# Optimization experiments

Measured on AMD Instinct MI355X. Metric: run time of the kernel, lower is better.

Reference implementation:

```python
import jax, jax.numpy as jnp
import numpy as np

B, C, N, H = 4, 512, 2048, 8
D = C // H  # per-head depth = 64
EPS = 1e-5


def conv1x1(x, W, b):
    # x: [B, Cin, N], W: [Cout, Cin], b: [Cout]
    return jnp.einsum('oc,bcn->bon', W, x) + b[None, :, None]


def instance_norm(x):
    # normalize over length dim per (batch, channel), no affine
    mu = jnp.mean(x, axis=-1, keepdims=True)
    var = jnp.var(x, axis=-1, keepdims=True)
    return (x - mu) * jax.lax.rsqrt(var + EPS)


def _pipeline(src, tgt, Wq, bq, Wk, bk, Wv, bv, Wm, bm):
    # query from src, key/value from tgt; reshape C -> (D outer, H inner)
    q = conv1x1(src, Wq, bq).reshape(B, D, H, N)
    k = conv1x1(tgt, Wk, bk).reshape(B, D, H, N)
    v = conv1x1(tgt, Wv, bv).reshape(B, D, H, N)
    scores = jnp.einsum('bdhn,bdhm->bhnm', q, k) / jnp.sqrt(jnp.float32(D))
    probs = jax.nn.softmax(scores, axis=-1)
    out = jnp.einsum('bhnm,bdhm->bdhn', probs, v).reshape(B, C, N)
    return conv1x1(out, Wm, bm)


def _mlp(x, W1, b1, W2, b2):
    h = conv1x1(x, W1, b1)
    h = jax.nn.relu(instance_norm(h))
    return conv1x1(h, W2, b2)


def setup_inputs() -> dict:
    key = jax.random.key(0)
    ks = jax.random.split(key, 8)
    s = 0.02
    return {
        'source_features': jax.random.normal(ks[0], (B, C, N), jnp.float32),
        'target_features': jax.random.normal(ks[1], (B, C, N), jnp.float32),
        'Wq': jax.random.normal(ks[2], (C, C), jnp.float32) * s,
        'bq': jnp.zeros((C,), jnp.float32),
        'Wk': jax.random.normal(ks[3], (C, C), jnp.float32) * s,
        'bk': jnp.zeros((C,), jnp.float32),
        'Wv': jax.random.normal(ks[4], (C, C), jnp.float32) * s,
        'bv': jnp.zeros((C,), jnp.float32),
        'Wm': jax.random.normal(ks[5], (C, C), jnp.float32) * s,
        'bm': jnp.zeros((C,), jnp.float32),
        'W1': jax.random.normal(ks[6], (2 * C, 2 * C), jnp.float32) * s,
        'b1': jnp.zeros((2 * C,), jnp.float32),
        'W2': jax.random.normal(ks[7], (C, 2 * C), jnp.float32) * s,
        'b2': jnp.zeros((C,), jnp.float32),
    }


def reference(source_features, target_features, Wq, bq, Wk, bk, Wv, bv, Wm, bm, W1, b1, W2, b2):
    src, tgt = source_features, target_features
    # source update uses ORIGINAL target features
    src_att = _pipeline(src, tgt, Wq, bq, Wk, bk, Wv, bv, Wm, bm)
    src = src + _mlp(jnp.concatenate([src, src_att], axis=1), W1, b1, W2, b2)
    # target update uses the UPDATED source features (in-place semantics of original)
    tgt_att = _pipeline(tgt, src, Wq, bq, Wk, bk, Wv, bv, Wm, bm)
    tgt = tgt + _mlp(jnp.concatenate([tgt, tgt_att], axis=1), W1, b1, W2, b2)
    return src, tgt
```

## Files before the change

### kernel.cpp

```cpp
#include <hip/hip_runtime.h>

#define NN 2048
#define CC 512
#define BB 4
#define HH 8
#define DD 64
#define SCALE 0.18033688011112043f

typedef unsigned short u16;
typedef __attribute__((ext_vector_type(8))) short bf16x8;
typedef __attribute__((ext_vector_type(4))) float f32x4;

extern "C" __device__ float __ocml_exp2_f32(float);

__device__ inline u16 f2b(float x) {
    unsigned u = __builtin_bit_cast(unsigned, x);
    u += 0x7fffu + ((u >> 16) & 1u);
    return (u16)(u >> 16);
}
__device__ inline float b2f(u16 h) {
    unsigned u = ((unsigned)h) << 16;
    return __builtin_bit_cast(float, u);
}

#define GLD16(g, l) __builtin_amdgcn_global_load_lds( \
    (const __attribute__((address_space(1))) unsigned int*)(g), \
    (__attribute__((address_space(3))) unsigned int*)(l), 16, 0, 0)

template<int JT>
__device__ __forceinline__ void gemm_core_t(
    const u16* __restrict__ Xa, const u16* __restrict__ Xb, int Ca, int K,
    const u16* __restrict__ Wt, size_t rowBase,
    u16* As, u16* Bs, f32x4 (&acc)[4][JT])
{
    constexpr int OT = JT * 32;
    const int tid = threadIdx.x;
    const int lane = tid & 63, w = tid >> 6;
    const int quad = lane >> 4, l16 = lane & 15;
    const int wrow = w & 1, wcol = w >> 1;
    const int arow = lane >> 2, aseg = lane & 3;

    for (int k0 = 0; k0 < K; k0 += 32) {
        const u16* Xs; int Crow, cc;
        if (k0 < Ca) { Xs = Xa; Crow = Ca; cc = k0; }
        else         { Xs = Xb; Crow = K - Ca; cc = k0 - Ca; }
#pragma unroll
        for (int i = 0; i < 2; ++i) {
            int rl = w * 32 + i * 16 + arow;
            int la = __builtin_amdgcn_readfirstlane((w * 32 + i * 16) * 32);
            GLD16(Xs + (rowBase + rl) * (size_t)Crow + cc + aseg * 8, (char*)As + (size_t)la * 2);
        }
#pragma unroll
        for (int i = 0; i < OT / 64; ++i) {
            int rl = w * (OT / 4) + i * 16 + arow;
            int la = __builtin_amdgcn_readfirstlane((w * (OT / 4) + i * 16) * 32);
            GLD16(Wt + (size_t)rl * K + k0 + aseg * 8, (char*)Bs + (size_t)la * 2);
        }
        __syncthreads();
        bf16x8 av[4], bv[JT];
#pragma unroll
        for (int i = 0; i < 4; ++i)
            av[i] = *(const bf16x8*)&As[(wrow * 64 + i * 16 + l16) * 32 + quad * 8];
#pragma unroll
        for (int jj = 0; jj < JT; ++jj)
            bv[jj] = *(const bf16x8*)&Bs[(wcol * JT * 16 + jj * 16 + l16) * 32 + quad * 8];
#pragma unroll
        for (int i = 0; i < 4; ++i)
#pragma unroll
            for (int jj = 0; jj < JT; ++jj)
                acc[i][jj] = __builtin_amdgcn_mfma_f32_16x16x32_bf16(av[i], bv[jj], acc[i][jj], 0, 0, 0);
        __syncthreads();
    }
}

template<int JT>
__device__ __forceinline__ void gemm_epilogue_t(
    f32x4 (&acc)[4][JT], const float* __restrict__ bias, int mode,
    int b, int n0, int o0, int Cout,
    const float* __restrict__ res, float* __restrict__ outF, u16* __restrict__ outB)
{
    const int tid = threadIdx.x;
    const int lane = tid & 63, w = tid >> 6;
    const int quad = lane >> 4, l16 = lane & 15;
    const int wrow = w & 1, wcol = w >> 1;
    const size_t bN = (size_t)b * NN;
    const int nb0 = n0 + wrow * 64, ob0 = o0 + wcol * JT * 16;

    if (mode == 0) {
#pragma unroll
        for (int j = 0; j < JT; ++j) {
            int o = ob0 + j * 16 + l16;
            float bs = bias[o];
#pragma unroll
            for (int i = 0; i < 4; ++i)
#pragma unroll
                for (int r = 0; r < 4; ++r) {
                    int n = nb0 + i * 16 + quad * 4 + r;
                    outB[(bN + n) * Cout + o] = f2b(acc[i][j][r] + bs);
                }
        }
    } else if (mode == 1) {
#pragma unroll
        for (int j = 0; j < JT; ++j) {
            int o = ob0 + j * 16 + l16;
            float bs = bias[o];
            int h = o >> 6, d = o & 63;
#pragma unroll
            for (int i = 0; i < 4; ++i) {
                int n = nb0 + i * 16 + quad * 4;
                ushort4 pk;
                pk.x = f2b(acc[i][j][0] + bs); pk.y = f2b(acc[i][j][1] + bs);
                pk.z = f2b(acc[i][j][2] + bs); pk.w = f2b(acc[i][j][3] + bs);
                *(ushort4*)&outB[(((size_t)b * HH + h) * DD + d) * NN + n] = pk;
            }
        }
    } else {
#pragma unroll
        for (int j = 0; j < JT; ++j) {
            int o = ob0 + j * 16 + l16;
            float bs = bias[o];
#pragma unroll
            for (int i = 0; i < 4; ++i) {
                int n = nb0 + i * 16 + quad * 4;
                size_t ad = ((size_t)b * Cout + o) * NN + n;
                float4 rv = *(const float4*)&res[ad];
                float4 yv;
                yv.x = acc[i][j][0] + bs + rv.x;
                yv.y = acc[i][j][1] + bs + rv.y;
                yv.z = acc[i][j][2] + bs + rv.z;
                yv.w = acc[i][j][3] + bs + rv.w;
                *(float4*)&outF[ad] = yv;
                if (mode == 2) {
                    outB[(bN + n + 0) * Cout + o] = f2b(yv.x);
                    outB[(bN + n + 1) * Cout + o] = f2b(yv.y);
                    outB[(bN + n + 2) * Cout + o] = f2b(yv.z);
                    outB[(bN + n + 3) * Cout + o] = f2b(yv.w);
                }
            }
        }
    }
}

template<int JT>
__global__ __launch_bounds__(256, (JT == 2 ? 4 : 3)) void gemm_bf16_t(
    const u16* __restrict__ Wb, const float* __restrict__ bias,
    const u16* __restrict__ Xa, const u16* __restrict__ Xb,
    int Ca, int K, int Cout,
    const float* __restrict__ res, float* __restrict__ outF,
    u16* __restrict__ outB, int mode)
{
    __shared__ u16 As[128 * 32];
    __shared__ u16 Bs[JT * 32 * 32];
    const int b = blockIdx.z, n0 = blockIdx.x * 128, o0 = blockIdx.y * (JT * 32);
    f32x4 acc[4][JT] = {};
    gemm_core_t<JT>(Xa, Xb, Ca, K, Wb + (size_t)o0 * K, (size_t)b * NN + n0, As, Bs, acc);
    gemm_epilogue_t<JT>(acc, bias, mode, b, n0, o0, Cout, res, outF, outB);
}

__global__ __launch_bounds__(256, 3) void gemm_qkv(
    const u16* __restrict__ WQ, const float* __restrict__ bQ,
    const u16* __restrict__ XQ, u16* __restrict__ outQ,
    const u16* __restrict__ WK, const float* __restrict__ bK, u16* __restrict__ outK,
    const u16* __restrict__ WV, const float* __restrict__ bV, u16* __restrict__ outV,
    const u16* __restrict__ XKV)
{
    __shared__ u16 As[128 * 32];
    __shared__ u16 Bs[128 * 32];
    const int yb = blockIdx.y;
    const u16* W; const float* bias; const u16* X; u16* outB; int mode, o0;
    if (yb < 4)      { o0 = yb * 128;       W = WQ; bias = bQ; X = XQ;  outB = outQ; mode = 0; }
    else if (yb < 8) { o0 = (yb - 4) * 128; W = WK; bias = bK; X = XKV; outB = outK; mode = 0; }
    else             { o0 = (yb - 8) * 128; W = WV; bias = bV; X = XKV; outB = outV; mode = 1; }
    const int b = blockIdx.z, n0 = blockIdx.x * 128;
    f32x4 acc[4][4] = {};
    gemm_core_t<4>(X, nullptr, 512, 512, W + (size_t)o0 * 512, (size_t)b * NN + n0, As, Bs, acc);
    gemm_epilogue_t<4>(acc, bias, mode, b, n0, o0, 512, nullptr, nullptr, outB);
}

__global__ __launch_bounds__(256, 4) void attn(
    const u16* __restrict__ Qg, const u16* __restrict__ Kg,
    const u16* __restrict__ Vg, u16* __restrict__ Og)
{
    __shared__ __align__(16) u16 Ks[64 * 64];
    __shared__ __align__(16) u16 Vt[64 * 64];
    __shared__ __align__(16) u16 Ps[64 * 64];
    const int tid = threadIdx.x;
    const int lane = tid & 63, w = tid >> 6;
    const int quad = lane >> 4, l16 = lane & 15;
    const int id = blockIdx.x;
    const int xcd = id & 7, jj = id >> 3;
    const int bh = xcd * 4 + (jj >> 5), nb = jj & 31;
    const int b = bh >> 3, h = bh & 7;
    const int n0 = nb * 64, wn0 = w * 16;
    const size_t qkBase = ((size_t)b * NN) * CC + h * DD;
    const size_t vBase  = (((size_t)b * HH + h) * DD) * NN;
    const int r8 = lane >> 3, seg = lane & 7;
    const int lk = l16 & 7;

    bf16x8 qf[2];
    {
        int n = n0 + wn0 + l16;
#pragma unroll
        for (int ks = 0; ks < 2; ++ks)
            qf[ks] = *(const bf16x8*)&Qg[qkBase + (size_t)n * CC + ks * 32 + quad * 8];
    }

    const short oneb = 0x3F80;
    const bf16x8 ones = {oneb, oneb, oneb, oneb, oneb, oneb, oneb, oneb};
    f32x4 oa[4] = {};
    f32x4 lacc = {};

    for (int m0 = 0; m0 < NN; m0 += 64) {
#pragma unroll
        for (int it = 0; it < 2; ++it) {
            int rowb = w * 16 + it * 8;
            int segp = seg ^ r8;
            GLD16(&Kg[qkBase + (size_t)(m0 + rowb + r8) * CC + segp * 8], &Ks[rowb * 64]);
            GLD16(&Vg[vBase + (size_t)(rowb + r8) * NN + m0 + segp * 8], &Vt[rowb * 64]);
        }
        __syncthreads();

        f32x4 st[4] = {};
#pragma unroll
        for (int ks = 0; ks < 2; ++ks) {
            bf16x8 ak[4];
#pragma unroll
            for (int rt = 0; rt < 4; ++rt)
                ak[rt] = *(const bf16x8*)&Ks[(rt * 16 + l16) * 64 + ((ks * 4 + quad) ^ lk) * 8];
#pragma unroll
            for (int rt = 0; rt < 4; ++rt)
                st[rt] = __builtin_amdgcn_mfma_f32_16x16x32_bf16(ak[rt], qf[ks], st[rt], 0, 0, 0);
        }

        {
            int nrow = wn0 + l16;
#pragma unroll
            for (int rt = 0; rt < 4; ++rt) {
                unsigned u0 = __builtin_bit_cast(unsigned, __ocml_exp2_f32(st[rt][0]));
                unsigned u1 = __builtin_bit_cast(unsigned, __ocml_exp2_f32(st[rt][1]));
                unsigned u2 = __builtin_bit_cast(unsigned, __ocml_exp2_f32(st[rt][2]));
                unsigned u3 = __builtin_bit_cast(unsigned, __ocml_exp2_f32(st[rt][3]));
                uint2 t;
                t.x = __builtin_amdgcn_perm(u1, u0, 0x07060302u);
                t.y = __builtin_amdgcn_perm(u3, u2, 0x07060302u);
                int g = (rt * 2 + (quad >> 1)) ^ lk;
                *(uint2*)&Ps[nrow * 64 + g * 8 + (quad & 1) * 4] = t;
            }
        }

#pragma unroll
        for (int ks = 0; ks < 2; ++ks) {
            bf16x8 pa = *(const bf16x8*)&Ps[(wn0 + l16) * 64 + ((ks * 4 + quad) ^ lk) * 8];
            bf16x8 vb[4];
#pragma unroll
            for (int ct = 0; ct < 4; ++ct)
                vb[ct] = *(const bf16x8*)&Vt[(ct * 16 + l16) * 64 + ((ks * 4 + quad) ^ lk) * 8];
#pragma unroll
            for (int ct = 0; ct < 4; ++ct)
                oa[ct] = __builtin_amdgcn_mfma_f32_16x16x32_bf16(pa, vb[ct], oa[ct], 0, 0, 0);
            lacc = __builtin_amdgcn_mfma_f32_16x16x32_bf16(pa, ones, lacc, 0, 0, 0);
        }
        __syncthreads();
    }

#pragma unroll
    for (int r = 0; r < 4; ++r) {
        float li = 1.f / lacc[r];
        int n = n0 + wn0 + quad * 4 + r;
#pragma unroll
        for (int ct = 0; ct < 4; ++ct)
            Og[qkBase + (size_t)n * CC + ct * 16 + l16] = f2b(oa[ct][r] * li);
    }
}

__global__ __launch_bounds__(256) void transpose_cvt(
    const float* __restrict__ X, u16* __restrict__ Y)
{
    __shared__ float T[64][65];
    const int tid = threadIdx.x;
    const int n0 = blockIdx.x * 64, c0 = blockIdx.y * 64, b = blockIdx.z;
    const int rr = tid >> 4, cc4 = tid & 15;
#pragma unroll
    for (int p = 0; p < 4; ++p) {
        int cl = p * 16 + rr;
        float4 v = *(const float4*)&X[((size_t)b * CC + c0 + cl) * NN + n0 + cc4 * 4];
        T[cl][cc4 * 4 + 0] = v.x; T[cl][cc4 * 4 + 1] = v.y;
        T[cl][cc4 * 4 + 2] = v.z; T[cl][cc4 * 4 + 3] = v.w;
    }
    __syncthreads();
#pragma unroll
    for (int p = 0; p < 4; ++p) {
        int nl = p * 16 + rr;
        ushort4 pk;
        pk.x = f2b(T[cc4 * 4 + 0][nl]);
        pk.y = f2b(T[cc4 * 4 + 1][nl]);
        pk.z = f2b(T[cc4 * 4 + 2][nl]);
        pk.w = f2b(T[cc4 * 4 + 3][nl]);
        *(ushort4*)&Y[((size_t)b * NN + n0 + nl) * CC + c0 + cc4 * 4] = pk;
    }
}

__global__ __launch_bounds__(256) void prep_weights(
    const float* __restrict__ Wq, const float* __restrict__ Wk,
    const float* __restrict__ Wv, const float* __restrict__ Wm,
    const float* __restrict__ W1, const float* __restrict__ W2,
    u16* oQ, u16* oK, u16* oV, u16* oM, u16* o1, u16* o2)
{
    const float* W; u16* o; int rows, cols, perm; float sc = 1.f;
    switch (blockIdx.z) {
        case 0: W = Wq; o = oQ; rows = 512;  cols = 512;  perm = 1; sc = SCALE; break;
        case 1: W = Wk; o = oK; rows = 512;  cols = 512;  perm = 1; break;
        case 2: W = Wv; o = oV; rows = 512;  cols = 512;  perm = 1; break;
        case 3: W = Wm; o = oM; rows = 512;  cols = 512;  perm = 2; break;
        case 4: W = W1; o = o1; rows = 1024; cols = 1024; perm = 0; break;
        default: W = W2; o = o2; rows = 512; cols = 1024; perm = 0; break;
    }
    int c = blockIdx.x * 256 + threadIdx.x;
    int r = blockIdx.y;
    if (r >= rows || c >= cols) return;
    int sr = r, scol = c;
    if (perm == 1) sr = (r & 63) * 8 + (r >> 6);
    else if (perm == 2) scol = (c & 63) * 8 + (c >> 6);
    o[(size_t)r * cols + c] = f2b(W[(size_t)sr * cols + scol] * sc);
}

__global__ void prep_bias(const float* __restrict__ bq, const float* __restrict__ bk,
                          const float* __restrict__ bv,
                          float* oq, float* ok, float* ov)
{
    int i = blockIdx.x * 256 + threadIdx.x;
    int y = blockIdx.y;
    const float* s = (y == 0) ? bq : (y == 1) ? bk : bv;
    float* o = (y == 0) ? oq : (y == 1) ? ok : ov;
    float v = s[(i & 63) * 8 + (i >> 6)];
    if (y == 0) v *= SCALE;
    o[i] = v;
}

__global__ __launch_bounds__(256) void inorm_p1(
    const u16* __restrict__ X, float* __restrict__ Ssum, float* __restrict__ Ssq)
{
    __shared__ float rs[4][64], rq[4][64];
    const int tid = threadIdx.x;
    const int cl = tid & 63, g = tid >> 6;
    const int c = blockIdx.x * 64 + cl;
    const int b = blockIdx.y, nz = blockIdx.z;
    float s = 0.f, q = 0.f;
    size_t base = ((size_t)b * NN + nz * 256 + g * 64) * 1024 + c;
#pragma unroll 4
    for (int i = 0; i < 64; ++i) {
        float x = b2f(X[base + (size_t)i * 1024]);
        s += x; q += x * x;
    }
    rs[g][cl] = s; rq[g][cl] = q;
    __syncthreads();
    if (g == 0) {
        s = rs[0][cl] + rs[1][cl] + rs[2][cl] + rs[3][cl];
        q = rq[0][cl] + rq[1][cl] + rq[2][cl] + rq[3][cl];
        atomicAdd(&Ssum[b * 1024 + c], s);
        atomicAdd(&Ssq[b * 1024 + c], q);
    }
}

__global__ __launch_bounds__(256) void inorm_p2(
    u16* __restrict__ X, const float* __restrict__ Ssum, const float* __restrict__ Ssq)
{
    const int tid = threadIdx.x;
    const int cl = tid & 63, g = tid >> 6;
    const int c = blockIdx.x * 64 + cl;
    const int b = blockIdx.y, nz = blockIdx.z;
    float mean = Ssum[b * 1024 + c] * (1.f / NN);
    float var  = Ssq[b * 1024 + c] * (1.f / NN) - mean * mean;
    float rstd = rsqrtf(fmaxf(var, 0.f) + 1e-5f);
    size_t base = ((size_t)b * NN + nz * 256 + g * 64) * 1024 + c;
#pragma unroll 4
    for (int i = 0; i < 64; ++i) {
        float x = b2f(X[base + (size_t)i * 1024]);
        x = (x - mean) * rstd;
        X[base + (size_t)i * 1024] = f2b(fmaxf(x, 0.f));
    }
}

extern "C" void kernel_launch(void* const* d_in, const int* in_sizes, int n_in,
                              void* d_out, int out_size, void* d_ws, size_t ws_size,
                              hipStream_t stream)
{
    (void)in_sizes; (void)n_in; (void)out_size; (void)ws_size;
    const float* src = (const float*)d_in[0];
    const float* tgt = (const float*)d_in[1];
    const float* Wq = (const float*)d_in[2];  const float* bq = (const float*)d_in[3];
    const float* Wk = (const float*)d_in[4];  const float* bk = (const float*)d_in[5];
    const float* Wv = (const float*)d_in[6];  const float* bv = (const float*)d_in[7];
    const float* Wm = (const float*)d_in[8];  const float* bm = (const float*)d_in[9];
    const float* W1 = (const float*)d_in[10]; const float* b1 = (const float*)d_in[11];
    const float* W2 = (const float*)d_in[12]; const float* b2 = (const float*)d_in[13];

    char* w = (char*)d_ws;
    u16* WQp = (u16*)(w);
    u16* WKp = (u16*)(w + (512u << 10));
    u16* WVp = (u16*)(w + (1u << 20));
    u16* WMp = (u16*)(w + (3u << 19));
    u16* W1b = (u16*)(w + (2u << 20));
    u16* W2b = (u16*)(w + (4u << 20));
    float* BQp = (float*)(w + (5u << 20));
    float* BKp = BQp + 512;
    float* BVp = BQp + 1024;
    float* STS = BQp + 1536;
    float* STQ = STS + 4096;
    u16* X0 = (u16*)(w + ( 6u << 20));
    u16* X1 = (u16*)(w + (14u << 20));
    u16* B0 = (u16*)(w + (22u << 20));
    u16* B1 = (u16*)(w + (30u << 20));
    u16* B2 = (u16*)(w + (38u << 20));
    u16* B3 = (u16*)(w + (46u << 20));

    float* out = (float*)d_out;
    const size_t R = (size_t)BB * CC * NN;
    dim3 blk(256);

    prep_weights<<<dim3(4, 1024, 6), blk, 0, stream>>>(Wq, Wk, Wv, Wm, W1, W2,
                                                       WQp, WKp, WVp, WMp, W1b, W2b);
    prep_bias<<<dim3(2, 3), blk, 0, stream>>>(bq, bk, bv, BQp, BKp, BVp);
    transpose_cvt<<<dim3(32, 8, 4), blk, 0, stream>>>(src, X0);
    transpose_cvt<<<dim3(32, 8, 4), blk, 0, stream>>>(tgt, X1);

    dim3 gQKV(16, 12, 4), gM(16, 8, 4), gW1(16, 8, 4), gW2(16, 8, 4);

    gemm_qkv<<<gQKV, blk, 0, stream>>>(WQp, BQp, X0, B0, WKp, BKp, B1, WVp, BVp, B2, X1);
    attn<<<dim3(1024), blk, 0, stream>>>(B0, B1, B2, B3);
    gemm_bf16_t<2><<<gM, blk, 0, stream>>>(WMp, bm, B3, nullptr, 512, 512, 512, nullptr, nullptr, B0, 0);
    gemm_bf16_t<4><<<gW1, blk, 0, stream>>>(W1b, b1, X0, B0, 512, 1024, 1024, nullptr, nullptr, B1, 0);
    hipMemsetAsync(STS, 0, 8192 * sizeof(float), stream);
    inorm_p1<<<dim3(16, 4, 8), blk, 0, stream>>>(B1, STS, STQ);
    inorm_p2<<<dim3(16, 4, 8), blk, 0, stream>>>(B1, STS, STQ);
    gemm_bf16_t<2><<<gW2, blk, 0, stream>>>(W2b, b2, B1, nullptr, 1024, 1024, 512, src, out, B3, 2);

    gemm_qkv<<<gQKV, blk, 0, stream>>>(WQp, BQp, X1, X0, WKp, BKp, B0, WVp, BVp, B1, B3);
    attn<<<dim3(1024), blk, 0, stream>>>(X0, B0, B1, B2);
    gemm_bf16_t<2><<<gM, blk, 0, stream>>>(WMp, bm, B2, nullptr, 512, 512, 512, nullptr, nullptr, X0, 0);
    gemm_bf16_t<4><<<gW1, blk, 0, stream>>>(W1b, b1, X1, X0, 512, 1024, 1024, nullptr, nullptr, B0, 0);
    hipMemsetAsync(STS, 0, 8192 * sizeof(float), stream);
    inorm_p1<<<dim3(16, 4, 8), blk, 0, stream>>>(B0, STS, STQ);
    inorm_p2<<<dim3(16, 4, 8), blk, 0, stream>>>(B0, STS, STQ);
    gemm_bf16_t<2><<<gW2, blk, 0, stream>>>(W2b, b2, B0, nullptr, 1024, 1024, 512, tgt, out + R, nullptr, 3);
}
```

Before: 448.5 us.

## Stage GEMM epilogues through LDS for coalesced stores; widen attention per-wave tiles

The row-major bf16 GEMM outputs now swap MFMA operands so each lane holds contiguous output channels. Results are staged in a padded LDS tile and written out as 16-byte coalesced rows instead of scattered 2-byte stores. The V projection gets the same LDS staging for its head-major layout. Attention switches to 128-thread blocks where each wave handles 32 query rows, reusing the K/V fragments across two query tiles at the cost of more registers and fewer waves per block.

```diff
diff --git a/kernel.cpp b/kernel.cpp
--- a/kernel.cpp
+++ b/kernel.cpp
@@ -27,7 +27,7 @@
     (const __attribute__((address_space(1))) unsigned int*)(g), \
     (__attribute__((address_space(3))) unsigned int*)(l), 16, 0, 0)
 
-template<int JT>
+template<int JT, bool SWAP>
 __device__ __forceinline__ void gemm_core_t(
     const u16* __restrict__ Xa, const u16* __restrict__ Xb, int Ca, int K,
     const u16* __restrict__ Wt, size_t rowBase,
@@ -68,93 +68,141 @@
         for (int i = 0; i < 4; ++i)
 #pragma unroll
             for (int jj = 0; jj < JT; ++jj)
-                acc[i][jj] = __builtin_amdgcn_mfma_f32_16x16x32_bf16(av[i], bv[jj], acc[i][jj], 0, 0, 0);
+                acc[i][jj] = SWAP
+                    ? __builtin_amdgcn_mfma_f32_16x16x32_bf16(bv[jj], av[i], acc[i][jj], 0, 0, 0)
+                    : __builtin_amdgcn_mfma_f32_16x16x32_bf16(av[i], bv[jj], acc[i][jj], 0, 0, 0);
         __syncthreads();
     }
 }
 
 template<int JT>
-__device__ __forceinline__ void gemm_epilogue_t(
-    f32x4 (&acc)[4][JT], const float* __restrict__ bias, int mode,
-    int b, int n0, int o0, int Cout,
-    const float* __restrict__ res, float* __restrict__ outF, u16* __restrict__ outB)
-{
+__device__ __forceinline__ void epi_nc(
+    f32x4 (&acc)[4][JT], const float* __restrict__ bias,
+    int b, int n0, int o0, int Cout, u16* __restrict__ outB, u16* T)
+{
+    constexpr int OT = JT * 32, SP = OT + 4;
     const int tid = threadIdx.x;
     const int lane = tid & 63, w = tid >> 6;
     const int quad = lane >> 4, l16 = lane & 15;
     const int wrow = w & 1, wcol = w >> 1;
     const size_t bN = (size_t)b * NN;
-    const int nb0 = n0 + wrow * 64, ob0 = o0 + wcol * JT * 16;
-
-    if (mode == 0) {
-#pragma unroll
-        for (int j = 0; j < JT; ++j) {
-            int o = ob0 + j * 16 + l16;
-            float bs = bias[o];
-#pragma unroll
-            for (int i = 0; i < 4; ++i)
-#pragma unroll
-                for (int r = 0; r < 4; ++r) {
-                    int n = nb0 + i * 16 + quad * 4 + r;
-                    outB[(bN + n) * Cout + o] = f2b(acc[i][j][r] + bs);
-                }
-        }
-    } else if (mode == 1) {
-#pragma unroll
-        for (int j = 0; j < JT; ++j) {
-            int o = ob0 + j * 16 + l16;
-            float bs = bias[o];
-            int h = o >> 6, d = o & 63;
-#pragma unroll
-            for (int i = 0; i < 4; ++i) {
-                int n = nb0 + i * 16 + quad * 4;
-                ushort4 pk;
-                pk.x = f2b(acc[i][j][0] + bs); pk.y = f2b(acc[i][j][1] + bs);
-                pk.z = f2b(acc[i][j][2] + bs); pk.w = f2b(acc[i][j][3] + bs);
-                *(ushort4*)&outB[(((size_t)b * HH + h) * DD + d) * NN + n] = pk;
-            }
-        }
-    } else {
-#pragma unroll
-        for (int j = 0; j < JT; ++j) {
-            int o = ob0 + j * 16 + l16;
-            float bs = bias[o];
-#pragma unroll
-            for (int i = 0; i < 4; ++i) {
-                int n = nb0 + i * 16 + quad * 4;
-                size_t ad = ((size_t)b * Cout + o) * NN + n;
-                float4 rv = *(const float4*)&res[ad];
-                float4 yv;
-                yv.x = acc[i][j][0] + bs + rv.x;
-                yv.y = acc[i][j][1] + bs + rv.y;
-                yv.z = acc[i][j][2] + bs + rv.z;
-                yv.w = acc[i][j][3] + bs + rv.w;
-                *(float4*)&outF[ad] = yv;
-                if (mode == 2) {
-                    outB[(bN + n + 0) * Cout + o] = f2b(yv.x);
-                    outB[(bN + n + 1) * Cout + o] = f2b(yv.y);
-                    outB[(bN + n + 2) * Cout + o] = f2b(yv.z);
-                    outB[(bN + n + 3) * Cout + o] = f2b(yv.w);
-                }
-            }
-        }
+
+#pragma unroll
+    for (int j = 0; j < JT; ++j) {
+        int ob = wcol * JT * 16 + j * 16 + quad * 4;
+        float4 b4;
+        b4.x = bias[o0 + ob + 0]; b4.y = bias[o0 + ob + 1];
+        b4.z = bias[o0 + ob + 2]; b4.w = bias[o0 + ob + 3];
+#pragma unroll
+        for (int i = 0; i < 4; ++i) {
+            int nt = wrow * 64 + i * 16 + l16;
+            ushort4 pk;
+            pk.x = f2b(acc[i][j][0] + b4.x); pk.y = f2b(acc[i][j][1] + b4.y);
+            pk.z = f2b(acc[i][j][2] + b4.z); pk.w = f2b(acc[i][j][3] + b4.w);
+            *(ushort4*)&T[nt * SP + ob] = pk;
+        }
+    }
+    __syncthreads();
+    constexpr int ROWB = OT * 2;
+    constexpr int RNDS = 128 * ROWB / 4096;
+#pragma unroll
+    for (int rnd = 0; rnd < RNDS; ++rnd) {
+        int linear = rnd * 4096 + tid * 16;
+        int nt = linear / ROWB, off = linear % ROWB;
+        uint4 v = *(uint4*)&T[nt * SP + off / 2];
+        *(uint4*)((char*)&outB[(bN + n0 + nt) * Cout + o0] + off) = v;
+    }
+}
+
+__device__ __forceinline__ void epi_v(
+    f32x4 (&acc)[4][4], const float* __restrict__ bias,
+    int b, int n0, int o0, u16* __restrict__ outB, u16* T)
+{
+    const int tid = threadIdx.x;
+    const int lane = tid & 63, w = tid >> 6;
+    const int quad = lane >> 4, l16 = lane & 15;
+    const int wrow = w & 1, wcol = w >> 1;
+
+#pragma unroll
+    for (int j = 0; j < 4; ++j) {
+        int ot = wcol * 64 + j * 16 + l16;
+        float bs = bias[o0 + ot];
+#pragma unroll
+        for (int i = 0; i < 4; ++i) {
+            int nt = wrow * 64 + i * 16 + quad * 4;
+            ushort4 pk;
+            pk.x = f2b(acc[i][j][0] + bs); pk.y = f2b(acc[i][j][1] + bs);
+            pk.z = f2b(acc[i][j][2] + bs); pk.w = f2b(acc[i][j][3] + bs);
+            *(ushort4*)&T[ot * 136 + nt] = pk;
+        }
+    }
+    __syncthreads();
+#pragma unroll
+    for (int rnd = 0; rnd < 8; ++rnd) {
+        int linear = rnd * 4096 + tid * 16;
+        int ot = linear >> 8, off = linear & 255;
+        int o = o0 + ot, h = o >> 6, d = o & 63;
+        uint4 v = *(uint4*)&T[ot * 136 + off / 2];
+        *(uint4*)((char*)&outB[(((size_t)b * HH + h) * DD + d) * NN + n0] + off) = v;
     }
 }
 
 template<int JT>
-__global__ __launch_bounds__(256, (JT == 2 ? 4 : 3)) void gemm_bf16_t(
+__global__ __launch_bounds__(256, (JT == 2 ? 4 : 3)) void gemm_nc(
     const u16* __restrict__ Wb, const float* __restrict__ bias,
     const u16* __restrict__ Xa, const u16* __restrict__ Xb,
-    int Ca, int K, int Cout,
+    int Ca, int K, int Cout, u16* __restrict__ outB)
+{
+    constexpr int SZ = (JT == 2) ? (128 * 68) : (128 * 132);
+    __shared__ __align__(16) u16 smem[SZ];
+    u16* As = smem; u16* Bs = smem + 4096;
+    const int b = blockIdx.z, n0 = blockIdx.x * 128, o0 = blockIdx.y * (JT * 32);
+    f32x4 acc[4][JT] = {};
+    gemm_core_t<JT, true>(Xa, Xb, Ca, K, Wb + (size_t)o0 * K, (size_t)b * NN + n0, As, Bs, acc);
+    epi_nc<JT>(acc, bias, b, n0, o0, Cout, outB, smem);
+}
+
+__global__ __launch_bounds__(256, 4) void gemm_f(
+    const u16* __restrict__ Wb, const float* __restrict__ bias,
+    const u16* __restrict__ Xa, int K, int Cout,
     const float* __restrict__ res, float* __restrict__ outF,
     u16* __restrict__ outB, int mode)
 {
-    __shared__ u16 As[128 * 32];
-    __shared__ u16 Bs[JT * 32 * 32];
-    const int b = blockIdx.z, n0 = blockIdx.x * 128, o0 = blockIdx.y * (JT * 32);
-    f32x4 acc[4][JT] = {};
-    gemm_core_t<JT>(Xa, Xb, Ca, K, Wb + (size_t)o0 * K, (size_t)b * NN + n0, As, Bs, acc);
-    gemm_epilogue_t<JT>(acc, bias, mode, b, n0, o0, Cout, res, outF, outB);
+    __shared__ __align__(16) u16 smem[128 * 32 + 64 * 32];
+    u16* As = smem; u16* Bs = smem + 4096;
+    const int b = blockIdx.z, n0 = blockIdx.x * 128, o0 = blockIdx.y * 64;
+    f32x4 acc[4][2] = {};
+    gemm_core_t<2, false>(Xa, nullptr, K, K, Wb + (size_t)o0 * K, (size_t)b * NN + n0, As, Bs, acc);
+
+    const int tid = threadIdx.x;
+    const int lane = tid & 63, w = tid >> 6;
+    const int quad = lane >> 4, l16 = lane & 15;
+    const int wrow = w & 1, wcol = w >> 1;
+    const size_t bN = (size_t)b * NN;
+    const int nb0 = n0 + wrow * 64, ob0 = o0 + wcol * 32;
+#pragma unroll
+    for (int j = 0; j < 2; ++j) {
+        int o = ob0 + j * 16 + l16;
+        float bs = bias[o];
+#pragma unroll
+        for (int i = 0; i < 4; ++i) {
+            int n = nb0 + i * 16 + quad * 4;
+            size_t ad = ((size_t)b * Cout + o) * NN + n;
+            float4 rv = *(const float4*)&res[ad];
+            float4 yv;
+            yv.x = acc[i][j][0] + bs + rv.x;
+            yv.y = acc[i][j][1] + bs + rv.y;
+            yv.z = acc[i][j][2] + bs + rv.z;
+            yv.w = acc[i][j][3] + bs + rv.w;
+            *(float4*)&outF[ad] = yv;
+            if (mode == 2) {
+                outB[(bN + n + 0) * Cout + o] = f2b(yv.x);
+                outB[(bN + n + 1) * Cout + o] = f2b(yv.y);
+                outB[(bN + n + 2) * Cout + o] = f2b(yv.z);
+                outB[(bN + n + 3) * Cout + o] = f2b(yv.w);
+            }
+        }
+    }
 }
 
 __global__ __launch_bounds__(256, 3) void gemm_qkv(
@@ -164,20 +212,26 @@
     const u16* __restrict__ WV, const float* __restrict__ bV, u16* __restrict__ outV,
     const u16* __restrict__ XKV)
 {
-    __shared__ u16 As[128 * 32];
-    __shared__ u16 Bs[128 * 32];
+    __shared__ __align__(16) u16 smem[128 * 136];
+    u16* As = smem; u16* Bs = smem + 4096;
     const int yb = blockIdx.y;
-    const u16* W; const float* bias; const u16* X; u16* outB; int mode, o0;
-    if (yb < 4)      { o0 = yb * 128;       W = WQ; bias = bQ; X = XQ;  outB = outQ; mode = 0; }
-    else if (yb < 8) { o0 = (yb - 4) * 128; W = WK; bias = bK; X = XKV; outB = outK; mode = 0; }
-    else             { o0 = (yb - 8) * 128; W = WV; bias = bV; X = XKV; outB = outV; mode = 1; }
     const int b = blockIdx.z, n0 = blockIdx.x * 128;
-    f32x4 acc[4][4] = {};
-    gemm_core_t<4>(X, nullptr, 512, 512, W + (size_t)o0 * 512, (size_t)b * NN + n0, As, Bs, acc);
-    gemm_epilogue_t<4>(acc, bias, mode, b, n0, o0, 512, nullptr, nullptr, outB);
-}
-
-__global__ __launch_bounds__(256, 4) void attn(
+    if (yb < 8) {
+        const u16* W; const float* bias; const u16* X; u16* outB; int o0;
+        if (yb < 4) { o0 = yb * 128;       W = WQ; bias = bQ; X = XQ;  outB = outQ; }
+        else        { o0 = (yb - 4) * 128; W = WK; bias = bK; X = XKV; outB = outK; }
+        f32x4 acc[4][4] = {};
+        gemm_core_t<4, true>(X, nullptr, 512, 512, W + (size_t)o0 * 512, (size_t)b * NN + n0, As, Bs, acc);
+        epi_nc<4>(acc, bias, b, n0, o0, 512, outB, smem);
+    } else {
+        int o0 = (yb - 8) * 128;
+        f32x4 acc[4][4] = {};
+        gemm_core_t<4, false>(XKV, nullptr, 512, 512, WV + (size_t)o0 * 512, (size_t)b * NN + n0, As, Bs, acc);
+        epi_v(acc, bV, b, n0, o0, outV, smem);
+    }
+}
+
+__global__ __launch_bounds__(128, 2) void attn(
     const u16* __restrict__ Qg, const u16* __restrict__ Kg,
     const u16* __restrict__ Vg, u16* __restrict__ Og)
 {
@@ -191,36 +245,37 @@
     const int xcd = id & 7, jj = id >> 3;
     const int bh = xcd * 4 + (jj >> 5), nb = jj & 31;
     const int b = bh >> 3, h = bh & 7;
-    const int n0 = nb * 64, wn0 = w * 16;
+    const int n0 = nb * 64, wn0 = w * 32;
     const size_t qkBase = ((size_t)b * NN) * CC + h * DD;
     const size_t vBase  = (((size_t)b * HH + h) * DD) * NN;
     const int r8 = lane >> 3, seg = lane & 7;
     const int lk = l16 & 7;
 
-    bf16x8 qf[2];
-    {
-        int n = n0 + wn0 + l16;
+    bf16x8 qf[2][2];
+#pragma unroll
+    for (int ct = 0; ct < 2; ++ct) {
+        int n = n0 + wn0 + ct * 16 + l16;
 #pragma unroll
         for (int ks = 0; ks < 2; ++ks)
-            qf[ks] = *(const bf16x8*)&Qg[qkBase + (size_t)n * CC + ks * 32 + quad * 8];
+            qf[ct][ks] = *(const bf16x8*)&Qg[qkBase + (size_t)n * CC + ks * 32 + quad * 8];
     }
 
     const short oneb = 0x3F80;
     const bf16x8 ones = {oneb, oneb, oneb, oneb, oneb, oneb, oneb, oneb};
-    f32x4 oa[4] = {};
-    f32x4 lacc = {};
+    f32x4 oa[2][4] = {};
+    f32x4 lacc[2] = {};
 
     for (int m0 = 0; m0 < NN; m0 += 64) {
 #pragma unroll
-        for (int it = 0; it < 2; ++it) {
-            int rowb = w * 16 + it * 8;
+        for (int it = 0; it < 4; ++it) {
+            int rowb = wn0 + it * 8;
             int segp = seg ^ r8;
             GLD16(&Kg[qkBase + (size_t)(m0 + rowb + r8) * CC + segp * 8], &Ks[rowb * 64]);
             GLD16(&Vg[vBase + (size_t)(rowb + r8) * NN + m0 + segp * 8], &Vt[rowb * 64]);
         }
         __syncthreads();
 
-        f32x4 st[4] = {};
+        f32x4 st[4][2] = {};
 #pragma unroll
         for (int ks = 0; ks < 2; ++ks) {
             bf16x8 ak[4];
@@ -229,17 +284,20 @@
                 ak[rt] = *(const bf16x8*)&Ks[(rt * 16 + l16) * 64 + ((ks * 4 + quad) ^ lk) * 8];
 #pragma unroll
             for (int rt = 0; rt < 4; ++rt)
-                st[rt] = __builtin_amdgcn_mfma_f32_16x16x32_bf16(ak[rt], qf[ks], st[rt], 0, 0, 0);
-        }
-
-        {
-            int nrow = wn0 + l16;
+#pragma unroll
+                for (int ct = 0; ct < 2; ++ct)
+                    st[rt][ct] = __builtin_amdgcn_mfma_f32_16x16x32_bf16(ak[rt], qf[ct][ks], st[rt][ct], 0, 0, 0);
+        }
+
+#pragma unroll
+        for (int ct = 0; ct < 2; ++ct) {
+            int nrow = wn0 + ct * 16 + l16;
 #pragma unroll
             for (int rt = 0; rt < 4; ++rt) {
-                unsigned u0 = __builtin_bit_cast(unsigned, __ocml_exp2_f32(st[rt][0]));
-                unsigned u1 = __builtin_bit_cast(unsigned, __ocml_exp2_f32(st[rt][1]));
-                unsigned u2 = __builtin_bit_cast(unsigned, __ocml_exp2_f32(st[rt][2]));
-                unsigned u3 = __builtin_bit_cast(unsigned, __ocml_exp2_f32(st[rt][3]));
+                unsigned u0 = __builtin_bit_cast(unsigned, __ocml_exp2_f32(st[rt][ct][0]));
+                unsigned u1 = __builtin_bit_cast(unsigned, __ocml_exp2_f32(st[rt][ct][1]));
+                unsigned u2 = __builtin_bit_cast(unsigned, __ocml_exp2_f32(st[rt][ct][2]));
+                unsigned u3 = __builtin_bit_cast(unsigned, __ocml_exp2_f32(st[rt][ct][3]));
                 uint2 t;
                 t.x = __builtin_amdgcn_perm(u1, u0, 0x07060302u);
                 t.y = __builtin_amdgcn_perm(u3, u2, 0x07060302u);
@@ -250,27 +308,32 @@
 
 #pragma unroll
         for (int ks = 0; ks < 2; ++ks) {
-            bf16x8 pa = *(const bf16x8*)&Ps[(wn0 + l16) * 64 + ((ks * 4 + quad) ^ lk) * 8];
             bf16x8 vb[4];
 #pragma unroll
-            for (int ct = 0; ct < 4; ++ct)
-                vb[ct] = *(const bf16x8*)&Vt[(ct * 16 + l16) * 64 + ((ks * 4 + quad) ^ lk) * 8];
-#pragma unroll
-            for (int ct = 0; ct < 4; ++ct)
-                oa[ct] = __builtin_amdgcn_mfma_f32_16x16x32_bf16(pa, vb[ct], oa[ct], 0, 0, 0);
-            lacc = __builtin_amdgcn_mfma_f32_16x16x32_bf16(pa, ones, lacc, 0, 0, 0);
+            for (int dt = 0; dt < 4; ++dt)
+                vb[dt] = *(const bf16x8*)&Vt[(dt * 16 + l16) * 64 + ((ks * 4 + quad) ^ lk) * 8];
+#pragma unroll
+            for (int ct = 0; ct < 2; ++ct) {
+                bf16x8 pa = *(const bf16x8*)&Ps[(wn0 + ct * 16 + l16) * 64 + ((ks * 4 + quad) ^ lk) * 8];
+#pragma unroll
+                for (int dt = 0; dt < 4; ++dt)
+                    oa[ct][dt] = __builtin_amdgcn_mfma_f32_16x16x32_bf16(pa, vb[dt], oa[ct][dt], 0, 0, 0);
+                lacc[ct] = __builtin_amdgcn_mfma_f32_16x16x32_bf16(pa, ones, lacc[ct], 0, 0, 0);
+            }
         }
         __syncthreads();
     }
 
 #pragma unroll
-    for (int r = 0; r < 4; ++r) {
-        float li = 1.f / lacc[r];
-        int n = n0 + wn0 + quad * 4 + r;
-#pragma unroll
-        for (int ct = 0; ct < 4; ++ct)
-            Og[qkBase + (size_t)n * CC + ct * 16 + l16] = f2b(oa[ct][r] * li);
-    }
+    for (int ct = 0; ct < 2; ++ct)
+#pragma unroll
+        for (int r = 0; r < 4; ++r) {
+            float li = 1.f / lacc[ct][r];
+            int n = n0 + wn0 + ct * 16 + quad * 4 + r;
+#pragma unroll
+            for (int dt = 0; dt < 4; ++dt)
+                Og[qkBase + (size_t)n * CC + dt * 16 + l16] = f2b(oa[ct][dt][r] * li);
+        }
 }
 
 __global__ __launch_bounds__(256) void transpose_cvt(
@@ -427,20 +490,20 @@
     dim3 gQKV(16, 12, 4), gM(16, 8, 4), gW1(16, 8, 4), gW2(16, 8, 4);
 
     gemm_qkv<<<gQKV, blk, 0, stream>>>(WQp, BQp, X0, B0, WKp, BKp, B1, WVp, BVp, B2, X1);
-    attn<<<dim3(1024), blk, 0, stream>>>(B0, B1, B2, B3);
-    gemm_bf16_t<2><<<gM, blk, 0, stream>>>(WMp, bm, B3, nullptr, 512, 512, 512, nullptr, nullptr, B0, 0);
-    gemm_bf16_t<4><<<gW1, blk, 0, stream>>>(W1b, b1, X0, B0, 512, 1024, 1024, nullptr, nullptr, B1, 0);
+    attn<<<dim3(1024), dim3(128), 0, stream>>>(B0, B1, B2, B3);
+    gemm_nc<2><<<gM, blk, 0, stream>>>(WMp, bm, B3, nullptr, 512, 512, 512, B0);
+    gemm_nc<4><<<gW1, blk, 0, stream>>>(W1b, b1, X0, B0, 512, 1024, 1024, B1);
     hipMemsetAsync(STS, 0, 8192 * sizeof(float), stream);
     inorm_p1<<<dim3(16, 4, 8), blk, 0, stream>>>(B1, STS, STQ);
     inorm_p2<<<dim3(16, 4, 8), blk, 0, stream>>>(B1, STS, STQ);
-    gemm_bf16_t<2><<<gW2, blk, 0, stream>>>(W2b, b2, B1, nullptr, 1024, 1024, 512, src, out, B3, 2);
+    gemm_f<<<gW2, blk, 0, stream>>>(W2b, b2, B1, 1024, 512, src, out, B3, 2);
 
     gemm_qkv<<<gQKV, blk, 0, stream>>>(WQp, BQp, X1, X0, WKp, BKp, B0, WVp, BVp, B1, B3);
-    attn<<<dim3(1024), blk, 0, stream>>>(X0, B0, B1, B2);
-    gemm_bf16_t<2><<<gM, blk, 0, stream>>>(WMp, bm, B2, nullptr, 512, 512, 512, nullptr, nullptr, X0, 0);
-    gemm_bf16_t<4><<<gW1, blk, 0, stream>>>(W1b, b1, X1, X0, 512, 1024, 1024, nullptr, nullptr, B0, 0);
+    attn<<<dim3(1024), dim3(128), 0, stream>>>(X0, B0, B1, B2);
+    gemm_nc<2><<<gM, blk, 0, stream>>>(WMp, bm, B2, nullptr, 512, 512, 512, X0);
+    gemm_nc<4><<<gW1, blk, 0, stream>>>(W1b, b1, X1, X0, 512, 1024, 1024, B0);
     hipMemsetAsync(STS, 0, 8192 * sizeof(float), stream);
     inorm_p1<<<dim3(16, 4, 8), blk, 0, stream>>>(B0, STS, STQ);
     inorm_p2<<<dim3(16, 4, 8), blk, 0, stream>>>(B0, STS, STQ);
-    gemm_bf16_t<2><<<gW2, blk, 0, stream>>>(W2b, b2, B0, nullptr, 1024, 1024, 512, tgt, out + R, nullptr, 3);
-}
+    gemm_f<<<gW2, blk, 0, stream>>>(W2b, b2, B0, 1024, 512, tgt, out + R, nullptr, 3);
+}
```

Result: no change. 453.3 us (+1.1%).
